# Kernel optimization log

Measured on AMD Instinct MI355X. Metric: run time of the kernel, lower is better.

Reference implementation:

```python
import jax, jax.numpy as jnp
import numpy as np

B, S, H, E, V, EXTRA = 128, 512, 1024, 1024, 50000, 500
EPS = 1e-8


def setup_inputs() -> dict:
    key = jax.random.key(0)
    ks = jax.random.split(key, 32)
    sc = 0.02
    n = lambda k, sh: (jax.random.normal(k, sh, jnp.float32) * sc)
    return {
        'inputs': jax.random.randint(ks[0], (B, 1), 0, V),
        'dec_hidden': n(ks[1], (1, B, H)),
        'enc_outputs': n(ks[2], (B, S, H)),
        'enc_padding_mask': jnp.zeros((B, S), jnp.float32),
        'context_vector_t1': n(ks[3], (B, H)),
        'enc_batch_extend_vocab': jax.random.randint(ks[4], (B, S), 0, V + EXTRA),
        'extra_zeros': jnp.zeros((B, EXTRA), jnp.float32),
        'coverage': jax.random.uniform(ks[5], (B, S), jnp.float32) * 0.1,
        # parameters
        'embed': n(ks[6], (V, E)),
        'ln_g': jnp.ones((E,), jnp.float32),
        'ln_b': jnp.zeros((E,), jnp.float32),
        'xc_W': n(ks[7], (E, H + E)), 'xc_b': jnp.zeros((E,), jnp.float32),
        'W_ih': n(ks[8], (3 * H, E)), 'W_hh': n(ks[9], (3 * H, H)),
        'b_ih': jnp.zeros((3 * H,), jnp.float32), 'b_hh': jnp.zeros((3 * H,), jnp.float32),
        'Wh': n(ks[10], (H, H)),
        'Ws': n(ks[11], (H, H)), 'Ws_b': jnp.zeros((H,), jnp.float32),
        'Wc': n(ks[12], (H, 1)),
        'Vv': n(ks[13], (H,)),
        'pg_W': n(ks[14], (2 * H + E,)), 'pg_b': jnp.zeros((1,), jnp.float32),
        'out1_W': n(ks[15], (H, 2 * H)), 'out1_b': jnp.zeros((H,), jnp.float32),
        'out2_W': n(ks[16], (V, H)), 'out2_b': jnp.zeros((V,), jnp.float32),
    }


def _layernorm(x, g, b):
    mu = jnp.mean(x, axis=-1, keepdims=True)
    var = jnp.mean(jnp.square(x - mu), axis=-1, keepdims=True)
    return (x - mu) / jnp.sqrt(var + 1e-5) * g + b


def reference(inputs, dec_hidden, enc_outputs, enc_padding_mask, context_vector_t1,
              enc_batch_extend_vocab, extra_zeros, coverage,
              embed, ln_g, ln_b, xc_W, xc_b, W_ih, W_hh, b_ih, b_hh,
              Wh, Ws, Ws_b, Wc, Vv, pg_W, pg_b, out1_W, out1_b, out2_W, out2_b):
    # embedding + layernorm: [B, E]
    x = _layernorm(embed[inputs[:, 0]], ln_g, ln_b)
    # x_context: Linear(H+E -> E)
    x = jnp.concatenate([x, context_vector_t1], axis=1) @ xc_W.T + xc_b

    # single GRU step (torch gate order r, z, n)
    h0 = dec_hidden[0]  # [B, H]
    gx = x @ W_ih.T + b_ih
    gh = h0 @ W_hh.T + b_hh
    r = jax.nn.sigmoid(gx[:, :H] + gh[:, :H])
    z = jax.nn.sigmoid(gx[:, H:2 * H] + gh[:, H:2 * H])
    nn_ = jnp.tanh(gx[:, 2 * H:] + r * gh[:, 2 * H:])
    s_t = (1.0 - z) * nn_ + z * h0  # [B, H]; dec_output == s_t for 1-layer GRU
    dec_output = s_t

    # Bahdanau additive attention with coverage
    enc_feat = jnp.einsum('bsh,kh->bsk', enc_outputs, Wh)           # [B,S,H]
    dec_feat = s_t @ Ws.T + Ws_b                                     # [B,H]
    cov_feat = coverage[:, :, None] * Wc[:, 0][None, None, :]        # [B,S,H]
    e_t = jnp.einsum('bsh,h->bs', jnp.tanh(enc_feat + dec_feat[:, None, :] + cov_feat), Vv)
    atten_dist = jax.nn.softmax(e_t + enc_padding_mask, axis=1)      # [B,S]
    h_t = jnp.einsum('bs,bsh->bh', atten_dist, enc_outputs)          # [B,H]
    coverage_next = coverage + atten_dist

    # pointer generator gate
    p_gen_in = jnp.concatenate([h_t, s_t, x], axis=1)                # [B, 2H+E]
    p_gen = jnp.clip(jax.nn.sigmoid(p_gen_in @ pg_W + pg_b), EPS, None)[:, None]  # [B,1]

    # vocab distribution
    s_t_h_t = jnp.concatenate([dec_output, h_t], axis=1)             # [B,2H]
    logits = (s_t_h_t @ out1_W.T + out1_b) @ out2_W.T + out2_b       # [B,V]
    vocab_dist = jax.nn.softmax(logits, axis=1)

    # mix + scatter-add copy distribution over extended vocab
    vocab_dist_ = jnp.concatenate([p_gen * vocab_dist, extra_zeros], axis=1)  # [B, V+EXTRA]
    atten_dist_ = (1.0 - p_gen) * atten_dist
    rows = jnp.arange(B)[:, None]
    final_dist = vocab_dist_.at[rows, enc_batch_extend_vocab].add(atten_dist_)
    final_dist = jnp.clip(final_dist, EPS, None)

    coverage_loss = jnp.sum(jnp.minimum(atten_dist, coverage_next), axis=1)  # [B]
    return (jnp.log(final_dist), s_t[None], h_t, coverage_next, coverage_loss)
```

## Files before the change

kernel.cpp:

```cpp
#include <hip/hip_runtime.h>
#include <hip/hip_bf16.h>
#include <stdint.h>

#define B_ 128
#define S_ 512
#define H_ 1024
#define E_ 1024
#define V_ 50000
#define EXTRA_ 500
#define VE_ 50500
#define EPS_ 1e-8f

typedef __attribute__((ext_vector_type(4))) float f32x4;
typedef __attribute__((ext_vector_type(8))) short bf16x8;

__device__ __forceinline__ unsigned short f2bf(float f) {
    unsigned u = __builtin_bit_cast(unsigned, f);
    u = (u + 0x7FFFu + ((u >> 16) & 1u)) >> 16;
    return (unsigned short)u;
}

__device__ __forceinline__ bf16x8 pack8(const float* f) {
    union { bf16x8 v; unsigned short s[8]; } u;
#pragma unroll
    for (int i = 0; i < 8; ++i) u.s[i] = f2bf(f[i]);
    return u.v;
}

__device__ __forceinline__ float bf2f(unsigned short s) {
    unsigned u = (unsigned)s << 16;
    return __builtin_bit_cast(float, u);
}

__device__ __forceinline__ float fast_tanh(float x) {
    x = fminf(fmaxf(x, -15.f), 15.f);
    float e = __expf(2.f * x);
    return __fdividef(e - 1.f, e + 1.f);
}

__device__ __forceinline__ void gload16(const void* g, void* l) {
    __builtin_amdgcn_global_load_lds(
        reinterpret_cast<const __attribute__((address_space(1))) unsigned int*>(
            reinterpret_cast<uintptr_t>(g)),
        reinterpret_cast<__attribute__((address_space(3))) unsigned int*>(
            reinterpret_cast<uintptr_t>(l)),
        16, 0, 0);
}

__global__ __launch_bounds__(256) void cvt_bf16_kernel(const float* __restrict__ in,
                                                       unsigned short* __restrict__ out) {
    int i = (blockIdx.x * 256 + threadIdx.x) * 8;
    float f[8];
    *(float4*)f     = *(const float4*)(in + i);
    *(float4*)(f+4) = *(const float4*)(in + i + 4);
    union { uint4 v; unsigned short s[8]; } u;
#pragma unroll
    for (int j = 0; j < 8; ++j) u.s[j] = f2bf(f[j]);
    *(uint4*)(out + i) = u.v;
}

__global__ __launch_bounds__(256) void embed_ln_kernel(
    const int* __restrict__ tok, const float* __restrict__ embed,
    const float* __restrict__ g, const float* __restrict__ beta,
    const float* __restrict__ ctx, float* __restrict__ x_cat)
{
    __shared__ float red[256];
    int b = blockIdx.x, t = threadIdx.x;
    const float* row = embed + (size_t)tok[b] * E_;
    float v[4];
    float s = 0.f;
#pragma unroll
    for (int i = 0; i < 4; ++i) { v[i] = row[t + i*256]; s += v[i]; }
    red[t] = s; __syncthreads();
    for (int o = 128; o > 0; o >>= 1) { if (t < o) red[t] += red[t+o]; __syncthreads(); }
    float mu = red[0] * (1.f/E_);
    __syncthreads();
    s = 0.f;
#pragma unroll
    for (int i = 0; i < 4; ++i) { float d = v[i]-mu; s += d*d; }
    red[t] = s; __syncthreads();
    for (int o = 128; o > 0; o >>= 1) { if (t < o) red[t] += red[t+o]; __syncthreads(); }
    float inv = rsqrtf(red[0]*(1.f/E_) + 1e-5f);
    float* xrow = x_cat + (size_t)b * 2048;
#pragma unroll
    for (int i = 0; i < 4; ++i) {
        int j = t + i*256;
        xrow[j] = (v[i]-mu)*inv*g[j] + beta[j];
        xrow[1024 + j] = ctx[b*1024 + j];
    }
}

__global__ __launch_bounds__(256) void gemm128_kernel(
    const float* __restrict__ A, const float* __restrict__ W,
    const float* __restrict__ bias, float* __restrict__ C,
    int N, int K, int ldc, int kchunk)
{
    __shared__ char Ab[128*64*2];
    __shared__ char Wb[64*64*2];
    const int t = threadIdx.x;
    const int wid = t >> 6, lane = t & 63;
    const int waveM = wid >> 1, waveN = wid & 1;
    const int lq = lane >> 4, lr = lane & 15;
    const int n0 = blockIdx.x * 64;
    const int kbeg = blockIdx.y * kchunk, kend = kbeg + kchunk;
    f32x4 acc[4][2];
#pragma unroll
    for (int i = 0; i < 4; ++i)
#pragma unroll
        for (int j = 0; j < 2; ++j) acc[i][j] = (f32x4){0.f,0.f,0.f,0.f};
    for (int kc = kbeg; kc < kend; kc += 64) {
        __syncthreads();
#pragma unroll
        for (int i = 0; i < 4; ++i) {
            int c = t + i*256;
            int row = c >> 3, k8 = (c & 7) << 3;
            const float* src = A + (size_t)row*K + kc + k8;
            float f[8];
            *(float4*)f     = *(const float4*)src;
            *(float4*)(f+4) = *(const float4*)(src+4);
            int byte = row*128 + ((k8*2) ^ ((row&7)<<4));
            *(bf16x8*)(Ab + byte) = pack8(f);
        }
#pragma unroll
        for (int i = 0; i < 2; ++i) {
            int c = t + i*256;
            int row = c >> 3, k8 = (c & 7) << 3;
            int n = n0 + row;
            float f[8] = {0,0,0,0,0,0,0,0};
            if (n < N) {
                const float* src = W + (size_t)n*K + kc + k8;
                *(float4*)f     = *(const float4*)src;
                *(float4*)(f+4) = *(const float4*)(src+4);
            }
            int byte = row*128 + ((k8*2) ^ ((row&7)<<4));
            *(bf16x8*)(Wb + byte) = pack8(f);
        }
        __syncthreads();
#pragma unroll
        for (int kf = 0; kf < 2; ++kf) {
            int kk2 = (kf*32 + (lq<<3)) * 2;
            bf16x8 bfr[2];
#pragma unroll
            for (int nf = 0; nf < 2; ++nf) {
                int r = waveN*32 + nf*16 + lr;
                bfr[nf] = *(const bf16x8*)(Wb + r*128 + (kk2 ^ ((r&7)<<4)));
            }
#pragma unroll
            for (int mf = 0; mf < 4; ++mf) {
                int r = waveM*64 + mf*16 + lr;
                bf16x8 afr = *(const bf16x8*)(Ab + r*128 + (kk2 ^ ((r&7)<<4)));
#pragma unroll
                for (int nf = 0; nf < 2; ++nf)
                    acc[mf][nf] = __builtin_amdgcn_mfma_f32_16x16x32_bf16(afr, bfr[nf], acc[mf][nf], 0, 0, 0);
            }
        }
    }
    float* Cp = C + (size_t)blockIdx.y * 128 * (size_t)ldc;
    bool addb = (bias != nullptr) && (blockIdx.y == 0);
#pragma unroll
    for (int mf = 0; mf < 4; ++mf)
#pragma unroll
        for (int nf = 0; nf < 2; ++nf) {
            int n = n0 + waveN*32 + nf*16 + lr;
            if (n < N) {
                float bv = addb ? bias[n] : 0.f;
#pragma unroll
                for (int r = 0; r < 4; ++r) {
                    int m = waveM*64 + mf*16 + (lq<<2) + r;
                    Cp[(size_t)m*ldc + n] = acc[mf][nf][r] + bv;
                }
            }
        }
}

__global__ __launch_bounds__(256) void reduce4_kernel(
    const float* __restrict__ in, float* __restrict__ out, int len)
{
    int i = blockIdx.x*256 + threadIdx.x;
    if (i < len) out[i] = in[i] + in[len+i] + in[2*len+i] + in[3*len+i];
}

__global__ __launch_bounds__(256) void gru_gate_kernel(
    const float* __restrict__ gxp, const float* __restrict__ ghp,
    const float* __restrict__ h0, float* __restrict__ s_t)
{
    int i = blockIdx.x*256 + threadIdx.x;
    int b = i >> 10, h = i & 1023;
    const float* gx0 = gxp + (size_t)b*3072;
    const float* gx1 = gx0 + 393216;
    const float* gh0 = ghp + (size_t)b*3072;
    const float* gh1 = gh0 + 393216;
    float grx = gx0[h] + gx1[h],        grh = gh0[h] + gh1[h];
    float gzx = gx0[h+1024]+gx1[h+1024], gzh = gh0[h+1024]+gh1[h+1024];
    float gnx = gx0[h+2048]+gx1[h+2048], gnh = gh0[h+2048]+gh1[h+2048];
    float r = 1.f/(1.f+__expf(-(grx + grh)));
    float z = 1.f/(1.f+__expf(-(gzx + gzh)));
    float n = fast_tanh(gnx + r*gnh);
    s_t[i] = (1.f-z)*n + z*h0[i];
}

__global__ __launch_bounds__(256,4) void attn_gemm_bf16_kernel(
    const unsigned short* __restrict__ encb,
    const unsigned short* __restrict__ whb,
    const float* __restrict__ ds_part,
    const float* __restrict__ coverage,
    const float* __restrict__ Wc, const float* __restrict__ Vv,
    float* __restrict__ e_part)
{
    __shared__ char Ab[128*128];
    __shared__ char Bb[128*128];
    const int t = threadIdx.x;
    const int wid = t >> 6, lane = t & 63;
    const int waveM = wid >> 1, waveN = wid & 1;
    const int lq = lane >> 4, lr = lane & 15;
    int bid = blockIdx.x;
    int wg = (bid & 7) * 512 + (bid >> 3);
    const int nt = wg & 7, mt = wg >> 3;
    const int m0 = mt * 128, n0 = nt * 128;
    const int b = m0 >> 9;

    const int grow = wid*8 + (lane >> 3);
    const int gk16 = (lane & 7) ^ ((lane >> 3) & 7);
    const unsigned short* asrc = encb + (size_t)(m0 + grow)*H_ + gk16*8;
    const unsigned short* bsrc = whb  + (size_t)(n0 + grow)*H_ + gk16*8;
    char* aldst = Ab + wid*1024;
    char* bldst = Bb + wid*1024;

    f32x4 acc[4][4];
#pragma unroll
    for (int i = 0; i < 4; ++i)
#pragma unroll
        for (int j = 0; j < 4; ++j) acc[i][j] = (f32x4){0.f,0.f,0.f,0.f};

    for (int kc = 0; kc < 1024; kc += 64) {
        __syncthreads();
#pragma unroll
        for (int i = 0; i < 4; ++i) {
            gload16(asrc + kc + i*32*H_, aldst + i*4096);
            gload16(bsrc + kc + i*32*H_, bldst + i*4096);
        }
        __syncthreads();
#pragma unroll
        for (int kf = 0; kf < 2; ++kf) {
            const int koff = kf*64 + lq*16;
            bf16x8 bfr[4];
#pragma unroll
            for (int nf = 0; nf < 4; ++nf) {
                int r = waveN*64 + nf*16 + lr;
                bfr[nf] = *(const bf16x8*)(Bb + r*128 + (koff ^ ((r&7)<<4)));
            }
#pragma unroll
            for (int mf = 0; mf < 4; ++mf) {
                int r = waveM*64 + mf*16 + lr;
                bf16x8 afr = *(const bf16x8*)(Ab + r*128 + (koff ^ ((r&7)<<4)));
#pragma unroll
                for (int nf = 0; nf < 4; ++nf)
                    acc[mf][nf] = __builtin_amdgcn_mfma_f32_16x16x32_bf16(afr, bfr[nf], acc[mf][nf], 0, 0, 0);
            }
        }
    }
    float cv[4][4];
#pragma unroll
    for (int mf = 0; mf < 4; ++mf)
#pragma unroll
        for (int r = 0; r < 4; ++r) {
            int m = m0 + waveM*64 + mf*16 + lq*4 + r;
            cv[mf][r] = coverage[b*S_ + (m & 511)];
        }
    float e_acc[4][4] = {};
#pragma unroll
    for (int nf = 0; nf < 4; ++nf) {
        int n = n0 + waveN*64 + nf*16 + lr;
        const float* dsp = ds_part + b*H_ + n;
        float df = dsp[0] + dsp[131072] + dsp[262144] + dsp[393216];
        float wc = Wc[n];
        float vv = Vv[n];
#pragma unroll
        for (int mf = 0; mf < 4; ++mf)
#pragma unroll
            for (int r = 0; r < 4; ++r)
                e_acc[mf][r] += fast_tanh(acc[mf][nf][r] + df + cv[mf][r]*wc) * vv;
    }
#pragma unroll
    for (int msk = 1; msk < 16; msk <<= 1)
#pragma unroll
        for (int mf = 0; mf < 4; ++mf)
#pragma unroll
            for (int r = 0; r < 4; ++r)
                e_acc[mf][r] += __shfl_xor(e_acc[mf][r], msk);
    __syncthreads();
    float* el = (float*)Ab;
    if (lr == 0) {
#pragma unroll
        for (int mf = 0; mf < 4; ++mf)
#pragma unroll
            for (int r = 0; r < 4; ++r)
                el[waveN*128 + waveM*64 + mf*16 + lq*4 + r] = e_acc[mf][r];
    }
    __syncthreads();
    if (t < 128)
        e_part[(size_t)nt*65536 + m0 + t] = el[t] + el[128 + t];
}

__global__ __launch_bounds__(512,4) void attn_gemm_f32_kernel(
    const float* __restrict__ enc, const float* __restrict__ Wh,
    const float* __restrict__ ds_part, const float* __restrict__ coverage,
    const float* __restrict__ Wc, const float* __restrict__ Vv,
    float* __restrict__ e_part)
{
    __shared__ char Ab[128*64*2];
    __shared__ char Bb[256*64*2];
    __shared__ float e_lds[4][128];
    const int t = threadIdx.x;
    const int wid = t >> 6, lane = t & 63;
    const int waveM = wid >> 2, waveN = wid & 3;
    const int lq = lane >> 4, lr = lane & 15;
    int bid = blockIdx.x;
    int wg = (bid & 7) * 256 + (bid >> 3);
    const int mt = wg >> 2, nt = wg & 3;
    const int m0 = mt * 128, n0 = nt * 256;
    const int b = m0 >> 9;
    const int arow = t >> 2, ak0 = (t & 3) * 16;
    const int brow = t >> 1, bk0 = (t & 1) * 32;
    f32x4 acc[4][4];
#pragma unroll
    for (int i = 0; i < 4; ++i)
#pragma unroll
        for (int j = 0; j < 4; ++j) acc[i][j] = (f32x4){0.f,0.f,0.f,0.f};
    for (int kc = 0; kc < 1024; kc += 64) {
        __syncthreads();
        {
            const float* src = enc + (size_t)(m0 + arow)*H_ + kc + ak0;
            float f[16];
            *(float4*)(f)    = *(const float4*)(src);
            *(float4*)(f+4)  = *(const float4*)(src+4);
            *(float4*)(f+8)  = *(const float4*)(src+8);
            *(float4*)(f+12) = *(const float4*)(src+12);
            char* dst = Ab + arow*128;
            int sw = (arow & 7) << 4;
            *(bf16x8*)(dst + ((ak0*2)      ^ sw)) = pack8(f);
            *(bf16x8*)(dst + ((ak0*2 + 16) ^ sw)) = pack8(f+8);
        }
        {
            const float* src = Wh + (size_t)(n0 + brow)*H_ + kc + bk0;
            char* dst = Bb + brow*128;
            int sw = (brow & 7) << 4;
            float f[16];
            *(float4*)(f)    = *(const float4*)(src);
            *(float4*)(f+4)  = *(const float4*)(src+4);
            *(float4*)(f+8)  = *(const float4*)(src+8);
            *(float4*)(f+12) = *(const float4*)(src+12);
            *(bf16x8*)(dst + ((bk0*2)      ^ sw)) = pack8(f);
            *(bf16x8*)(dst + ((bk0*2 + 16) ^ sw)) = pack8(f+8);
            *(float4*)(f)    = *(const float4*)(src+16);
            *(float4*)(f+4)  = *(const float4*)(src+20);
            *(float4*)(f+8)  = *(const float4*)(src+24);
            *(float4*)(f+12) = *(const float4*)(src+28);
            *(bf16x8*)(dst + ((bk0*2 + 32) ^ sw)) = pack8(f);
            *(bf16x8*)(dst + ((bk0*2 + 48) ^ sw)) = pack8(f+8);
        }
        __syncthreads();
#pragma unroll
        for (int kf = 0; kf < 2; ++kf) {
            const int koff = kf*64 + lq*16;
            bf16x8 bfr[4];
#pragma unroll
            for (int nf = 0; nf < 4; ++nf) {
                int r = waveN*64 + nf*16 + lr;
                bfr[nf] = *(const bf16x8*)(Bb + r*128 + (koff ^ ((r&7)<<4)));
            }
#pragma unroll
            for (int mf = 0; mf < 4; ++mf) {
                int r = waveM*64 + mf*16 + lr;
                bf16x8 afr = *(const bf16x8*)(Ab + r*128 + (koff ^ ((r&7)<<4)));
#pragma unroll
                for (int nf = 0; nf < 4; ++nf)
                    acc[mf][nf] = __builtin_amdgcn_mfma_f32_16x16x32_bf16(afr, bfr[nf], acc[mf][nf], 0, 0, 0);
            }
        }
    }
    float cv[4][4];
#pragma unroll
    for (int mf = 0; mf < 4; ++mf)
#pragma unroll
        for (int r = 0; r < 4; ++r) {
            int m = m0 + waveM*64 + mf*16 + lq*4 + r;
            cv[mf][r] = coverage[b*S_ + (m & 511)];
        }
    float e_acc[4][4] = {};
#pragma unroll
    for (int nf = 0; nf < 4; ++nf) {
        int n = n0 + waveN*64 + nf*16 + lr;
        const float* dsp = ds_part + b*H_ + n;
        float df = dsp[0] + dsp[131072] + dsp[262144] + dsp[393216];
        float wc = Wc[n];
        float vv = Vv[n];
#pragma unroll
        for (int mf = 0; mf < 4; ++mf)
#pragma unroll
            for (int r = 0; r < 4; ++r)
                e_acc[mf][r] += fast_tanh(acc[mf][nf][r] + df + cv[mf][r]*wc) * vv;
    }
#pragma unroll
    for (int msk = 1; msk < 16; msk <<= 1)
#pragma unroll
        for (int mf = 0; mf < 4; ++mf)
#pragma unroll
            for (int r = 0; r < 4; ++r)
                e_acc[mf][r] += __shfl_xor(e_acc[mf][r], msk);
    if (lr == 0) {
#pragma unroll
        for (int mf = 0; mf < 4; ++mf)
#pragma unroll
            for (int r = 0; r < 4; ++r)
                e_lds[waveN][waveM*64 + mf*16 + lq*4 + r] = e_acc[mf][r];
    }
    __syncthreads();
    if (t < 128)
        e_part[(size_t)nt*65536 + m0 + t] = e_lds[0][t] + e_lds[1][t] + e_lds[2][t] + e_lds[3][t];
}

__global__ __launch_bounds__(256) void attn_softmax_kernel(
    const float* __restrict__ e_part, int np, const float* __restrict__ mask,
    const float* __restrict__ cov, float* __restrict__ att,
    float* __restrict__ cov_next, float* __restrict__ loss)
{
    __shared__ float red[256];
    int b = blockIdx.x, t = threadIdx.x;
    int i1 = b*S_ + t, i2 = i1 + 256;
    float e1 = mask[i1], e2 = mask[i2];
    for (int p = 0; p < np; ++p) { e1 += e_part[(size_t)p*65536 + i1]; e2 += e_part[(size_t)p*65536 + i2]; }
    red[t] = fmaxf(e1, e2); __syncthreads();
    for (int o = 128; o > 0; o >>= 1) { if (t < o) red[t] = fmaxf(red[t], red[t+o]); __syncthreads(); }
    float m = red[0]; __syncthreads();
    float a1 = __expf(e1-m), a2 = __expf(e2-m);
    red[t] = a1+a2; __syncthreads();
    for (int o = 128; o > 0; o >>= 1) { if (t < o) red[t] += red[t+o]; __syncthreads(); }
    float inv = 1.f/red[0]; __syncthreads();
    a1 *= inv; a2 *= inv;
    att[i1] = a1; att[i2] = a2;
    float c1 = cov[i1]+a1, c2 = cov[i2]+a2;
    cov_next[i1] = c1; cov_next[i2] = c2;
    red[t] = fminf(a1,c1)+fminf(a2,c2); __syncthreads();
    for (int o = 128; o > 0; o >>= 1) { if (t < o) red[t] += red[t+o]; __syncthreads(); }
    if (t == 0) loss[b] = red[0];
}

__global__ __launch_bounds__(256) void context_part_bf16_kernel(
    const float* __restrict__ att, const unsigned short* __restrict__ encb, float* __restrict__ hq)
{
    __shared__ float asl[128];
    __shared__ float cpart[128][9];
    int b = blockIdx.x, q = blockIdx.y, t = threadIdx.x;
    if (t < 128) asl[t] = att[b*S_ + q*128 + t];
    __syncthreads();
    int lane = t & 127, su = t >> 7;
    int hc = lane * 8;
    const unsigned short* ep = encb + ((size_t)(b*S_ + q*128 + su*64))*H_ + hc;
    float acc[8] = {};
#pragma unroll 2
    for (int s = 0; s < 64; ++s) {
        uint4 v = *(const uint4*)(ep + (size_t)s*H_);
        float w = asl[su*64 + s];
        const unsigned short* pv = (const unsigned short*)&v;
#pragma unroll
        for (int k = 0; k < 8; ++k) acc[k] += w * bf2f(pv[k]);
    }
    if (su == 1) {
#pragma unroll
        for (int k = 0; k < 8; ++k) cpart[lane][k] = acc[k];
    }
    __syncthreads();
    if (su == 0) {
        float o[8];
#pragma unroll
        for (int k = 0; k < 8; ++k) o[k] = acc[k] + cpart[lane][k];
        float* dst = hq + (size_t)q*131072 + (size_t)b*1024 + hc;
        *(float4*)dst     = *(float4*)o;
        *(float4*)(dst+4) = *(float4*)(o+4);
    }
}

__global__ __launch_bounds__(256) void context_part_f32_kernel(
    const float* __restrict__ att, const float* __restrict__ enc, float* __restrict__ hq)
{
    __shared__ float asl[128];
    int b = blockIdx.x, sub = blockIdx.y;
    int hh = sub & 1, q = sub >> 1;
    int t = threadIdx.x;
    if (t < 128) asl[t] = att[b*S_ + q*128 + t];
    __syncthreads();
    int h = hh*512 + t*2;
    const float* ep = enc + (size_t)b*S_*H_ + (size_t)q*128*H_ + h;
    float a0 = 0.f, a1 = 0.f;
#pragma unroll 4
    for (int s = 0; s < 128; ++s) {
        float2 v = *(const float2*)(ep + (size_t)s*H_);
        float w = asl[s];
        a0 += w*v.x; a1 += w*v.y;
    }
    float* o = hq + ((size_t)q*B_ + b)*H_ + h;
    o[0] = a0; o[1] = a1;
}

__global__ __launch_bounds__(256) void pgen_kernel(
    const float* __restrict__ hq, const float* __restrict__ s_t, const float* __restrict__ x,
    const float* __restrict__ pgW, const float* __restrict__ pgb,
    float* __restrict__ pgen, float* __restrict__ h_t, float* __restrict__ A2)
{
    __shared__ float red[256];
    int b = blockIdx.x, t = threadIdx.x;
    float dot = 0.f;
#pragma unroll
    for (int i = 0; i < 4; ++i) {
        int j = t + i*256;
        const float* hp = hq + (size_t)b*1024 + j;
        float hv = hp[0] + hp[131072] + hp[262144] + hp[393216];
        float sv = s_t[b*1024 + j];
        h_t[b*1024 + j] = hv;
        A2[(size_t)b*2048 + j] = sv;
        A2[(size_t)b*2048 + 1024 + j] = hv;
        dot += hv*pgW[j] + sv*pgW[1024+j] + x[b*1024+j]*pgW[2048+j];
    }
    red[t] = dot; __syncthreads();
    for (int o = 128; o > 0; o >>= 1) { if (t < o) red[t] += red[t+o]; __syncthreads(); }
    if (t == 0) {
        float p = 1.f/(1.f+__expf(-(red[0] + pgb[0])));
        pgen[b] = fmaxf(p, EPS_);
    }
}

__global__ __launch_bounds__(256) void vocab_pass1_kernel(
    const float* __restrict__ logits, float2* __restrict__ mpart)
{
    __shared__ float rm[256], rl[256];
    int b = blockIdx.x, c = blockIdx.y, t = threadIdx.x;
    int lo = c * 12625;
    int hi = min(lo + 12625, V_);
    const float* row = logits + (size_t)b*VE_;
    float m = -1e30f, l = 0.f;
    for (int i = lo + t; i < hi; i += 256) {
        float v = row[i];
        if (v > m) { l = l*__expf(m-v) + 1.f; m = v; }
        else l += __expf(v-m);
    }
    rm[t] = m; rl[t] = l; __syncthreads();
    for (int o = 128; o > 0; o >>= 1) {
        if (t < o) {
            float m1 = rm[t], m2 = rm[t+o];
            float M = fmaxf(m1, m2);
            rl[t] = rl[t]*__expf(m1-M) + rl[t+o]*__expf(m2-M);
            rm[t] = M;
        }
        __syncthreads();
    }
    if (t == 0) mpart[b*4 + c] = make_float2(rm[0], rl[0]);
}

__global__ __launch_bounds__(256) void vocab_pass2_kernel(
    const float* __restrict__ logits, const float2* __restrict__ mpart,
    const float* __restrict__ pgen, const int* __restrict__ ebev,
    const float* __restrict__ att, float* __restrict__ out0)
{
    __shared__ unsigned bmap[395];
    __shared__ unsigned hkey[1024];
    __shared__ float hval[1024];
    int b = blockIdx.x, c = blockIdx.y, t = threadIdx.x;
    int lo = c * 12625, hi = lo + 12625;
    float2 p0 = mpart[b*4+0], p1 = mpart[b*4+1], p2 = mpart[b*4+2], p3 = mpart[b*4+3];
    float M = fmaxf(fmaxf(p0.x, p1.x), fmaxf(p2.x, p3.x));
    float L = p0.y*__expf(p0.x-M) + p1.y*__expf(p1.x-M) + p2.y*__expf(p2.x-M) + p3.y*__expf(p3.x-M);
    float pg = pgen[b];
    float inv = pg / L;
    for (int i = t; i < 395; i += 256) bmap[i] = 0u;
    for (int i = t; i < 1024; i += 256) { hkey[i] = 0xFFFFFFFFu; hval[i] = 0.f; }
    __syncthreads();
    for (int s = t; s < 512; s += 256) {
        int col = ebev[b*S_ + s];
        if (col >= lo && col < hi) {
            float v = (1.f - pg) * att[b*S_ + s];
            unsigned cl = (unsigned)(col - lo);
            atomicOr(&bmap[cl >> 5], 1u << (cl & 31));
            unsigned slot = (cl * 2654435761u >> 16) & 1023u;
            while (true) {
                unsigned old = atomicCAS(&hkey[slot], 0xFFFFFFFFu, cl);
                if (old == 0xFFFFFFFFu || old == cl) { atomicAdd(&hval[slot], v); break; }
                slot = (slot + 1) & 1023u;
            }
        }
    }
    __syncthreads();
    const float* row = logits + (size_t)b*VE_;
    float* orow = out0 + (size_t)b*VE_;
    for (int i = lo + t; i < hi; i += 256) {
        float base = 0.f;
        if (i < V_) base = __expf(row[i] - M) * inv;
        unsigned cl = (unsigned)(i - lo);
        if (bmap[cl >> 5] & (1u << (cl & 31))) {
            unsigned slot = (cl * 2654435761u >> 16) & 1023u;
            while (hkey[slot] != cl) slot = (slot + 1) & 1023u;
            base += hval[slot];
        }
        orow[i] = __logf(fmaxf(base, EPS_));
    }
}

extern "C" void kernel_launch(void* const* d_in, const int* in_sizes, int n_in,
                              void* d_out, int out_size, void* d_ws, size_t ws_size,
                              hipStream_t stream) {
    const int*   tok        = (const int*)d_in[0];
    const float* dec_hidden = (const float*)d_in[1];
    const float* enc        = (const float*)d_in[2];
    const float* mask       = (const float*)d_in[3];
    const float* ctx1       = (const float*)d_in[4];
    const int*   ebev       = (const int*)d_in[5];
    const float* cov        = (const float*)d_in[7];
    const float* embed      = (const float*)d_in[8];
    const float* ln_g       = (const float*)d_in[9];
    const float* ln_b       = (const float*)d_in[10];
    const float* xc_W       = (const float*)d_in[11];
    const float* xc_b       = (const float*)d_in[12];
    const float* W_ih       = (const float*)d_in[13];
    const float* W_hh       = (const float*)d_in[14];
    const float* b_ih       = (const float*)d_in[15];
    const float* b_hh       = (const float*)d_in[16];
    const float* Wh         = (const float*)d_in[17];
    const float* Ws         = (const float*)d_in[18];
    const float* Ws_b       = (const float*)d_in[19];
    const float* Wc         = (const float*)d_in[20];
    const float* Vv         = (const float*)d_in[21];
    const float* pg_W       = (const float*)d_in[22];
    const float* pg_b       = (const float*)d_in[23];
    const float* out1_W     = (const float*)d_in[24];
    const float* out1_b     = (const float*)d_in[25];
    const float* out2_W     = (const float*)d_in[26];
    const float* out2_b     = (const float*)d_in[27];

    float* out      = (float*)d_out;
    float* s_t      = out + 6464000;
    float* h_t      = out + 6595072;
    float* cov_next = out + 6726144;
    float* loss     = out + 6791680;

    const size_t ENC_SLOTS = 33554432, WH_SLOTS = 524288;
    const size_t BASE_SLOTS = 5178496;
    const size_t need = (ENC_SLOTS + WH_SLOTS + BASE_SLOTS) * 4;
    const bool bf16_path = (ws_size >= need);

    float* wsf = (float*)d_ws;
    unsigned short* enc_bf = (unsigned short*)d_ws;
    unsigned short* wh_bf  = (unsigned short*)(wsf + ENC_SLOTS);
    float* base     = bf16_path ? (wsf + ENC_SLOTS + WH_SLOTS) : wsf;
    float* x_cat    = base;
    float* x_part   = base + 262144;
    float* x        = base + 786432;
    float* gx_part  = base + 917504;
    float* gh_part  = base + 1703936;
    float* ds_part  = base + 2490368;
    float* e_part   = base + 3145728;
    float* att      = base + 3670016;
    float* pgen     = base + 3735552;
    float* A2       = base + 3735680;
    float* h2_part  = base + 3997824;
    float* h2       = base + 4522112;
    float* hq       = base + 4653184;
    float2* mpart   = (float2*)(base + 5177472);

    if (bf16_path) {
        cvt_bf16_kernel<<<32768, 256, 0, stream>>>(enc, enc_bf);
        cvt_bf16_kernel<<<512, 256, 0, stream>>>(Wh, wh_bf);
    }
    embed_ln_kernel<<<128, 256, 0, stream>>>(tok, embed, ln_g, ln_b, ctx1, x_cat);
    gemm128_kernel<<<dim3(16,4), 256, 0, stream>>>(x_cat, xc_W, xc_b, x_part, 1024, 2048, 1024, 512);
    reduce4_kernel<<<512, 256, 0, stream>>>(x_part, x, 131072);
    gemm128_kernel<<<dim3(48,2), 256, 0, stream>>>(x, W_ih, b_ih, gx_part, 3072, 1024, 3072, 512);
    gemm128_kernel<<<dim3(48,2), 256, 0, stream>>>(dec_hidden, W_hh, b_hh, gh_part, 3072, 1024, 3072, 512);
    gru_gate_kernel<<<512, 256, 0, stream>>>(gx_part, gh_part, dec_hidden, s_t);
    gemm128_kernel<<<dim3(16,4), 256, 0, stream>>>(s_t, Ws, Ws_b, ds_part, 1024, 1024, 1024, 256);

    int npart;
    if (bf16_path) {
        attn_gemm_bf16_kernel<<<4096, 256, 0, stream>>>(enc_bf, wh_bf, ds_part, cov, Wc, Vv, e_part);
        npart = 8;
    } else {
        attn_gemm_f32_kernel<<<2048, 512, 0, stream>>>(enc, Wh, ds_part, cov, Wc, Vv, e_part);
        npart = 4;
    }
    attn_softmax_kernel<<<128, 256, 0, stream>>>(e_part, npart, mask, cov, att, cov_next, loss);
    if (bf16_path) {
        dim3 g8(128, 4);
        context_part_bf16_kernel<<<g8, 256, 0, stream>>>(att, enc_bf, hq);
    } else {
        dim3 g8(128, 8);
        context_part_f32_kernel<<<g8, 256, 0, stream>>>(att, enc, hq);
    }
    pgen_kernel<<<128, 256, 0, stream>>>(hq, s_t, x, pg_W, pg_b, pgen, h_t, A2);
    gemm128_kernel<<<dim3(16,4), 256, 0, stream>>>(A2, out1_W, out1_b, h2_part, 1024, 2048, 1024, 512);
    reduce4_kernel<<<512, 256, 0, stream>>>(h2_part, h2, 131072);

    gemm128_kernel<<<dim3(782,1), 256, 0, stream>>>(h2, out2_W, out2_b, out, 50000, 1024, VE_, 1024);
    vocab_pass1_kernel<<<dim3(128,4), 256, 0, stream>>>(out, mpart);
    vocab_pass2_kernel<<<dim3(128,4), 256, 0, stream>>>(out, mpart, pgen, ebev, att, out);
}
```

Before: 528.6 us.

## Fold split-K partial sums into consumer loads and split vocab GEMM over K

Removes the reduce4 kernels by having the consuming GEMM sum the four split-K partials while loading its A tile, and pgen sums x partials directly. The large vocab-projection GEMM is split into two K halves (grid 782x2) writing a second partial buffer in workspace, and the two vocab softmax passes add both partials on read. This trades extra global reads (4x A loads in each GEMM block, second logit array) for fewer launches and more parallelism in the dominant out2 GEMM.

```diff
diff --git a/kernel.cpp b/kernel.cpp
--- a/kernel.cpp
+++ b/kernel.cpp
@@ -92,8 +92,8 @@
 
 __global__ __launch_bounds__(256) void gemm128_kernel(
     const float* __restrict__ A, const float* __restrict__ W,
-    const float* __restrict__ bias, float* __restrict__ C,
-    int N, int K, int ldc, int kchunk)
+    const float* __restrict__ bias, float* __restrict__ C, float* __restrict__ C1,
+    int N, int K, int ldc, int kchunk, int aparts)
 {
     __shared__ char Ab[128*64*2];
     __shared__ char Wb[64*64*2];
@@ -118,6 +118,16 @@
             float f[8];
             *(float4*)f     = *(const float4*)src;
             *(float4*)(f+4) = *(const float4*)(src+4);
+            if (aparts == 4) {
+#pragma unroll
+                for (int p = 1; p < 4; ++p) {
+                    float g0[8];
+                    *(float4*)g0     = *(const float4*)(src + p*131072);
+                    *(float4*)(g0+4) = *(const float4*)(src + p*131072 + 4);
+#pragma unroll
+                    for (int j = 0; j < 8; ++j) f[j] += g0[j];
+                }
+            }
             int byte = row*128 + ((k8*2) ^ ((row&7)<<4));
             *(bf16x8*)(Ab + byte) = pack8(f);
         }
@@ -155,7 +165,7 @@
             }
         }
     }
-    float* Cp = C + (size_t)blockIdx.y * 128 * (size_t)ldc;
+    float* Cp = (blockIdx.y == 0) ? C : (C1 + (size_t)(blockIdx.y - 1) * 128 * (size_t)ldc);
     bool addb = (bias != nullptr) && (blockIdx.y == 0);
 #pragma unroll
     for (int mf = 0; mf < 4; ++mf)
@@ -171,13 +181,6 @@
                 }
             }
         }
-}
-
-__global__ __launch_bounds__(256) void reduce4_kernel(
-    const float* __restrict__ in, float* __restrict__ out, int len)
-{
-    int i = blockIdx.x*256 + threadIdx.x;
-    if (i < len) out[i] = in[i] + in[len+i] + in[2*len+i] + in[3*len+i];
 }
 
 __global__ __launch_bounds__(256) void gru_gate_kernel(
@@ -504,7 +507,7 @@
 }
 
 __global__ __launch_bounds__(256) void pgen_kernel(
-    const float* __restrict__ hq, const float* __restrict__ s_t, const float* __restrict__ x,
+    const float* __restrict__ hq, const float* __restrict__ s_t, const float* __restrict__ x_part,
     const float* __restrict__ pgW, const float* __restrict__ pgb,
     float* __restrict__ pgen, float* __restrict__ h_t, float* __restrict__ A2)
 {
@@ -516,11 +519,13 @@
         int j = t + i*256;
         const float* hp = hq + (size_t)b*1024 + j;
         float hv = hp[0] + hp[131072] + hp[262144] + hp[393216];
+        const float* xp = x_part + (size_t)b*1024 + j;
+        float xv = xp[0] + xp[131072] + xp[262144] + xp[393216];
         float sv = s_t[b*1024 + j];
         h_t[b*1024 + j] = hv;
         A2[(size_t)b*2048 + j] = sv;
         A2[(size_t)b*2048 + 1024 + j] = hv;
-        dot += hv*pgW[j] + sv*pgW[1024+j] + x[b*1024+j]*pgW[2048+j];
+        dot += hv*pgW[j] + sv*pgW[1024+j] + xv*pgW[2048+j];
     }
     red[t] = dot; __syncthreads();
     for (int o = 128; o > 0; o >>= 1) { if (t < o) red[t] += red[t+o]; __syncthreads(); }
@@ -531,16 +536,19 @@
 }
 
 __global__ __launch_bounds__(256) void vocab_pass1_kernel(
-    const float* __restrict__ logits, float2* __restrict__ mpart)
+    const float* __restrict__ p0, const float* __restrict__ p1, int two,
+    float2* __restrict__ mpart)
 {
     __shared__ float rm[256], rl[256];
     int b = blockIdx.x, c = blockIdx.y, t = threadIdx.x;
     int lo = c * 12625;
     int hi = min(lo + 12625, V_);
-    const float* row = logits + (size_t)b*VE_;
+    const float* row = p0 + (size_t)b*VE_;
+    const float* row1 = two ? (p1 + (size_t)b*VE_) : row;
     float m = -1e30f, l = 0.f;
     for (int i = lo + t; i < hi; i += 256) {
         float v = row[i];
+        if (two) v += row1[i];
         if (v > m) { l = l*__expf(m-v) + 1.f; m = v; }
         else l += __expf(v-m);
     }
@@ -558,7 +566,8 @@
 }
 
 __global__ __launch_bounds__(256) void vocab_pass2_kernel(
-    const float* __restrict__ logits, const float2* __restrict__ mpart,
+    const float* __restrict__ p0, const float* __restrict__ p1, int two,
+    const float2* __restrict__ mpart,
     const float* __restrict__ pgen, const int* __restrict__ ebev,
     const float* __restrict__ att, float* __restrict__ out0)
 {
@@ -567,9 +576,9 @@
     __shared__ float hval[1024];
     int b = blockIdx.x, c = blockIdx.y, t = threadIdx.x;
     int lo = c * 12625, hi = lo + 12625;
-    float2 p0 = mpart[b*4+0], p1 = mpart[b*4+1], p2 = mpart[b*4+2], p3 = mpart[b*4+3];
-    float M = fmaxf(fmaxf(p0.x, p1.x), fmaxf(p2.x, p3.x));
-    float L = p0.y*__expf(p0.x-M) + p1.y*__expf(p1.x-M) + p2.y*__expf(p2.x-M) + p3.y*__expf(p3.x-M);
+    float2 q0 = mpart[b*4+0], q1 = mpart[b*4+1], q2 = mpart[b*4+2], q3 = mpart[b*4+3];
+    float M = fmaxf(fmaxf(q0.x, q1.x), fmaxf(q2.x, q3.x));
+    float L = q0.y*__expf(q0.x-M) + q1.y*__expf(q1.x-M) + q2.y*__expf(q2.x-M) + q3.y*__expf(q3.x-M);
     float pg = pgen[b];
     float inv = pg / L;
     for (int i = t; i < 395; i += 256) bmap[i] = 0u;
@@ -590,11 +599,16 @@
         }
     }
     __syncthreads();
-    const float* row = logits + (size_t)b*VE_;
+    const float* row = p0 + (size_t)b*VE_;
+    const float* row1 = two ? (p1 + (size_t)b*VE_) : row;
     float* orow = out0 + (size_t)b*VE_;
     for (int i = lo + t; i < hi; i += 256) {
         float base = 0.f;
-        if (i < V_) base = __expf(row[i] - M) * inv;
+        if (i < V_) {
+            float v = row[i];
+            if (two) v += row1[i];
+            base = __expf(v - M) * inv;
+        }
         unsigned cl = (unsigned)(i - lo);
         if (bmap[cl >> 5] & (1u << (cl & 31))) {
             unsigned slot = (cl * 2654435761u >> 16) & 1023u;
@@ -643,9 +657,12 @@
     float* loss     = out + 6791680;
 
     const size_t ENC_SLOTS = 33554432, WH_SLOTS = 524288;
-    const size_t BASE_SLOTS = 5178496;
-    const size_t need = (ENC_SLOTS + WH_SLOTS + BASE_SLOTS) * 4;
+    const size_t BASE_MIN  = 5178496;
+    const size_t BASE_SPLIT = 5178496 + 6464000;
+    const size_t need  = (ENC_SLOTS + WH_SLOTS + BASE_MIN) * 4;
+    const size_t need2 = (ENC_SLOTS + WH_SLOTS + BASE_SPLIT) * 4;
     const bool bf16_path = (ws_size >= need);
+    const bool split2 = bf16_path && (ws_size >= need2);
 
     float* wsf = (float*)d_ws;
     unsigned short* enc_bf = (unsigned short*)d_ws;
@@ -653,7 +670,6 @@
     float* base     = bf16_path ? (wsf + ENC_SLOTS + WH_SLOTS) : wsf;
     float* x_cat    = base;
     float* x_part   = base + 262144;
-    float* x        = base + 786432;
     float* gx_part  = base + 917504;
     float* gh_part  = base + 1703936;
     float* ds_part  = base + 2490368;
@@ -662,21 +678,20 @@
     float* pgen     = base + 3735552;
     float* A2       = base + 3735680;
     float* h2_part  = base + 3997824;
-    float* h2       = base + 4522112;
     float* hq       = base + 4653184;
     float2* mpart   = (float2*)(base + 5177472);
+    float* logit_p1 = base + 5178496;
 
     if (bf16_path) {
         cvt_bf16_kernel<<<32768, 256, 0, stream>>>(enc, enc_bf);
         cvt_bf16_kernel<<<512, 256, 0, stream>>>(Wh, wh_bf);
     }
     embed_ln_kernel<<<128, 256, 0, stream>>>(tok, embed, ln_g, ln_b, ctx1, x_cat);
-    gemm128_kernel<<<dim3(16,4), 256, 0, stream>>>(x_cat, xc_W, xc_b, x_part, 1024, 2048, 1024, 512);
-    reduce4_kernel<<<512, 256, 0, stream>>>(x_part, x, 131072);
-    gemm128_kernel<<<dim3(48,2), 256, 0, stream>>>(x, W_ih, b_ih, gx_part, 3072, 1024, 3072, 512);
-    gemm128_kernel<<<dim3(48,2), 256, 0, stream>>>(dec_hidden, W_hh, b_hh, gh_part, 3072, 1024, 3072, 512);
+    gemm128_kernel<<<dim3(16,4), 256, 0, stream>>>(x_cat, xc_W, xc_b, x_part, x_part + 131072, 1024, 2048, 1024, 512, 1);
+    gemm128_kernel<<<dim3(48,2), 256, 0, stream>>>(x_part, W_ih, b_ih, gx_part, gx_part + 393216, 3072, 1024, 3072, 512, 4);
+    gemm128_kernel<<<dim3(48,2), 256, 0, stream>>>(dec_hidden, W_hh, b_hh, gh_part, gh_part + 393216, 3072, 1024, 3072, 512, 1);
     gru_gate_kernel<<<512, 256, 0, stream>>>(gx_part, gh_part, dec_hidden, s_t);
-    gemm128_kernel<<<dim3(16,4), 256, 0, stream>>>(s_t, Ws, Ws_b, ds_part, 1024, 1024, 1024, 256);
+    gemm128_kernel<<<dim3(16,4), 256, 0, stream>>>(s_t, Ws, Ws_b, ds_part, ds_part + 131072, 1024, 1024, 1024, 256, 1);
 
     int npart;
     if (bf16_path) {
@@ -694,11 +709,16 @@
         dim3 g8(128, 8);
         context_part_f32_kernel<<<g8, 256, 0, stream>>>(att, enc, hq);
     }
-    pgen_kernel<<<128, 256, 0, stream>>>(hq, s_t, x, pg_W, pg_b, pgen, h_t, A2);
-    gemm128_kernel<<<dim3(16,4), 256, 0, stream>>>(A2, out1_W, out1_b, h2_part, 1024, 2048, 1024, 512);
-    reduce4_kernel<<<512, 256, 0, stream>>>(h2_part, h2, 131072);
-
-    gemm128_kernel<<<dim3(782,1), 256, 0, stream>>>(h2, out2_W, out2_b, out, 50000, 1024, VE_, 1024);
-    vocab_pass1_kernel<<<dim3(128,4), 256, 0, stream>>>(out, mpart);
-    vocab_pass2_kernel<<<dim3(128,4), 256, 0, stream>>>(out, mpart, pgen, ebev, att, out);
-}
+    pgen_kernel<<<128, 256, 0, stream>>>(hq, s_t, x_part, pg_W, pg_b, pgen, h_t, A2);
+    gemm128_kernel<<<dim3(16,4), 256, 0, stream>>>(A2, out1_W, out1_b, h2_part, h2_part + 131072, 1024, 2048, 1024, 512, 1);
+
+    if (split2) {
+        gemm128_kernel<<<dim3(782,2), 256, 0, stream>>>(h2_part, out2_W, out2_b, out, logit_p1, 50000, 1024, VE_, 512, 4);
+        vocab_pass1_kernel<<<dim3(128,4), 256, 0, stream>>>(out, logit_p1, 1, mpart);
+        vocab_pass2_kernel<<<dim3(128,4), 256, 0, stream>>>(out, logit_p1, 1, mpart, pgen, ebev, att, out);
+    } else {
+        gemm128_kernel<<<dim3(782,1), 256, 0, stream>>>(h2_part, out2_W, out2_b, out, nullptr, 50000, 1024, VE_, 1024, 4);
+        vocab_pass1_kernel<<<dim3(128,4), 256, 0, stream>>>(out, nullptr, 0, mpart);
+        vocab_pass2_kernel<<<dim3(128,4), 256, 0, stream>>>(out, nullptr, 0, mpart, pgen, ebev, att, out);
+    }
+}
```

New measurement: 570.2 us. +7.9%, slower.
